# Optimization experiments

Hardware: AMD Instinct MI355X
Metric: run time of the kernel (lower is better)

Reference implementation:

```python
import jax, jax.numpy as jnp
import numpy as np

K = 20          # args.k (minu=True)
EPS = 1e-5      # BatchNorm eps
BNS = float(1.0 / np.sqrt(1.0 + EPS))  # eval-mode BN with running_mean=0, running_var=1


def knn_idx(x, k):
    # x: (B, C, N); returns indices of k nearest neighbors (incl. self): (B, N, k)
    xx = jnp.sum(x * x, axis=1)                       # (B, N)
    inner = jnp.einsum('bcn,bcm->bnm', x, x)          # (B, N, N)
    dist = 2.0 * inner - xx[:, :, None] - xx[:, None, :]  # = -||xi - xj||^2
    return jax.lax.top_k(dist, k)[1]


def graph_feature(x, k):
    # x: (B, C, N) -> edge features (B, 2C, N, k) = cat(neighbor - center, center)
    idx = knn_idx(x, k)                               # (B, N, k)
    xt = jnp.transpose(x, (0, 2, 1))                  # (B, N, C)
    feat = jnp.take_along_axis(xt[:, None, :, :], idx[..., None], axis=2)  # (B, N, k, C)
    center = xt[:, :, None, :]
    out = jnp.concatenate([feat - center, jnp.broadcast_to(center, feat.shape)], axis=-1)
    return jnp.transpose(out, (0, 3, 1, 2))


def edge_block(x, w, g, b, k):
    # EdgeConv: gather -> 1x1 conv -> BN(eval) -> LeakyReLU(0.2) -> max over neighbors
    h = graph_feature(x, k)                           # (B, 2C, N, k)
    y = jnp.einsum('bcnk,oc->bonk', h, w)
    y = g[None, :, None, None] * (y * BNS) + b[None, :, None, None]
    y = jax.nn.leaky_relu(y, 0.2)
    return jnp.max(y, axis=-1)                        # (B, O, N)


def _bn1(v, g, b):
    return g * (v * BNS) + b


def setup_inputs() -> dict:
    key = jax.random.key(0)
    ks = jax.random.split(key, 32)
    B, C, N = 16, 6, 1024

    def w(k_, shape):
        return jax.random.normal(k_, shape, jnp.float32) / np.sqrt(shape[1])

    def gm(k_, n):
        return 1.0 + 0.1 * jax.random.normal(k_, (n,), jnp.float32)

    def bt(k_, n):
        return 0.1 * jax.random.normal(k_, (n,), jnp.float32)

    return {
        'x': jax.random.normal(ks[0], (B, C, N), jnp.float32),
        'disc': jax.random.normal(ks[1], (B, 1), jnp.float32),
        'w1': w(ks[2], (64, 12)),   'g1': gm(ks[3], 64),   'b1': bt(ks[4], 64),
        'w2': w(ks[5], (64, 128)),  'g2': gm(ks[6], 64),   'b2': bt(ks[7], 64),
        'w3': w(ks[8], (128, 128)), 'g3': gm(ks[9], 128),  'b3': bt(ks[10], 128),
        'w4': w(ks[11], (256, 256)),'g4': gm(ks[12], 256), 'b4': bt(ks[13], 256),
        'w5': w(ks[14], (1024, 512)),'g5': gm(ks[15], 1024),'b5': bt(ks[16], 1024),
        'wl1': w(ks[17], (256, 2048)),'g6': gm(ks[18], 256),'b6': bt(ks[19], 256),
        'wl2': w(ks[20], (128, 256)),'g7': gm(ks[21], 128),'b7': bt(ks[22], 128),
        'wl21': w(ks[23], (64, 128)),
        'wl22': w(ks[24], (32, 64)),'g8': gm(ks[25], 32), 'b8': bt(ks[26], 32),
        'wl3': w(ks[27], (90, 32)),
    }


def reference(x, disc, w1, g1, b1, w2, g2, b2, w3, g3, b3, w4, g4, b4,
              w5, g5, b5, wl1, g6, b6, wl2, g7, b7, wl21, wl22, g8, b8, wl3):
    # disc is accepted by the original forward but unused
    x1 = edge_block(x, w1, g1, b1, K)                 # (B, 64, N)
    x2 = edge_block(x1, w2, g2, b2, K)                # (B, 64, N)
    x3 = edge_block(x2, w3, g3, b3, K)                # (B, 128, N)
    x4 = edge_block(x3, w4, g4, b4, K)                # (B, 256, N)
    h = jnp.concatenate([x1, x2, x3, x4], axis=1)     # (B, 512, N)
    y = jnp.einsum('bcn,oc->bon', h, w5)              # conv5 1x1
    y = g5[None, :, None] * (y * BNS) + b5[None, :, None]
    y = jax.nn.leaky_relu(y, 0.2)                     # (B, emb, N)
    p = jnp.concatenate([jnp.max(y, axis=2), jnp.mean(y, axis=2)], axis=1)  # (B, 2*emb)
    z = jax.nn.leaky_relu(_bn1(p @ wl1.T, g6, b6), 0.2)
    z = jax.nn.leaky_relu(_bn1(z @ wl2.T, g7, b7), 0.2)
    z = jax.nn.gelu(_bn1((z @ wl21.T) @ wl22.T, g8, b8), approximate=False)
    return z @ wl3.T                                  # (B, 90)
```

## Files before the change

kernel.cpp:

```cpp
#include <hip/hip_runtime.h>
#include <math.h>
#include <float.h>

#define BNS_C 0.9999950000374996f

typedef __bf16 bf8 __attribute__((ext_vector_type(8)));
typedef float f4 __attribute__((ext_vector_type(4)));
union I4BF8 { int4 i; bf8 b; };

static __device__ __forceinline__ unsigned short f2bf(float f) {
    unsigned u = __float_as_uint(f);
    u += 0x7fff + ((u >> 16) & 1);
    return (unsigned short)(u >> 16);
}

__global__ void k_xin_t(const float* __restrict__ x, float* __restrict__ X0, float* __restrict__ xx) {
    int i = blockIdx.x * 256 + threadIdx.x;
    int b = i >> 10, n = i & 1023;
    const float* xb = x + (((size_t)b * 6) << 10) + n;
    float4* o4 = (float4*)(X0 + ((size_t)i << 3));
    float v0 = xb[0], v1 = xb[1 << 10], v2 = xb[2 << 10];
    float v3 = xb[3 << 10], v4 = xb[4 << 10], v5 = xb[5 << 10];
    o4[0] = make_float4(v0, v1, v2, v3);
    o4[1] = make_float4(v4, v5, 0.f, 0.f);
    xx[i] = v0*v0 + v1*v1 + v2*v2 + v3*v3 + v4*v4 + v5*v5;
}

__global__ __launch_bounds__(256) void k_gram2(const float* __restrict__ X, const float* __restrict__ xx,
                                               float* __restrict__ D, int Cp, int b0) {
    int z = blockIdx.z, b = b0 + z;
    int n0 = blockIdx.y * 64, m0 = blockIdx.x * 64;
    __shared__ float As[32 * 68], Bs[32 * 68];
    int tid = threadIdx.x;
    int ti = tid & 15, tj = tid >> 4;
    float acc[4][4] = {};
    const float* Xb = X + (((size_t)b) << 10) * Cp;
    for (int c0 = 0; c0 < Cp; c0 += 32) {
        for (int e = tid; e < 2048; e += 256) {
            int row = e >> 5, cc = e & 31, c = c0 + cc;
            float a = 0.f, bb = 0.f;
            if (c < Cp) {
                a  = Xb[(size_t)(n0 + row) * Cp + c];
                bb = Xb[(size_t)(m0 + row) * Cp + c];
            }
            As[cc * 68 + row] = a; Bs[cc * 68 + row] = bb;
        }
        __syncthreads();
#pragma unroll 8
        for (int cc = 0; cc < 32; ++cc) {
            const float4 av = *(const float4*)(As + cc * 68 + 4 * tj);
            const float4 bv = *(const float4*)(Bs + cc * 68 + 4 * ti);
            acc[0][0] += av.x * bv.x; acc[0][1] += av.x * bv.y; acc[0][2] += av.x * bv.z; acc[0][3] += av.x * bv.w;
            acc[1][0] += av.y * bv.x; acc[1][1] += av.y * bv.y; acc[1][2] += av.y * bv.z; acc[1][3] += av.y * bv.w;
            acc[2][0] += av.z * bv.x; acc[2][1] += av.z * bv.y; acc[2][2] += av.z * bv.z; acc[2][3] += av.z * bv.w;
            acc[3][0] += av.w * bv.x; acc[3][1] += av.w * bv.y; acc[3][2] += av.w * bv.z; acc[3][3] += av.w * bv.w;
        }
        __syncthreads();
    }
    const float4 xm = *(const float4*)(xx + (b << 10) + m0 + 4 * ti);
#pragma unroll
    for (int a = 0; a < 4; ++a) {
        int n = n0 + 4 * tj + a;
        float xn = xx[(b << 10) + n];
        float4 o;
        o.x = 2.f * acc[a][0] - xn - xm.x;
        o.y = 2.f * acc[a][1] - xn - xm.y;
        o.z = 2.f * acc[a][2] - xn - xm.z;
        o.w = 2.f * acc[a][3] - xn - xm.w;
        *(float4*)(D + ((size_t)((z << 10) + n) << 10) + m0 + 4 * ti) = o;
    }
}

__global__ __launch_bounds__(256) void k_topk(const float* __restrict__ D, int* __restrict__ idxo, int b0) {
    const int K = 20;
    int lane = threadIdx.x & 63;
    int rl = blockIdx.x * 4 + (threadIdx.x >> 6);
    const float* row = D + ((size_t)rl << 10);
    float d[16];
#pragma unroll
    for (int j = 0; j < 16; ++j) d[j] = row[lane + 64 * j];
    int rg = (b0 << 10) + rl;
    for (int it = 0; it < K; ++it) {
        float bv = d[0]; int bj = 0;
#pragma unroll
        for (int j = 1; j < 16; ++j) if (d[j] > bv) { bv = d[j]; bj = j; }
        int bm = lane + (bj << 6);
        for (int off = 32; off > 0; off >>= 1) {
            float ov = __shfl_down(bv, off);
            int   om = __shfl_down(bm, off);
            if (ov > bv || (ov == bv && om < bm)) { bv = ov; bm = om; }
        }
        bm = __shfl(bm, 0);
        if (lane == 0) idxo[rg * K + it] = bm;
        if ((bm & 63) == lane) d[bm >> 6] = -FLT_MAX;
    }
}

__global__ __launch_bounds__(256) void k_uv(const float* __restrict__ X, const float* __restrict__ w,
                                            float* __restrict__ V, float* __restrict__ U,
                                            int Cp, int C, int O) {
    int n0 = blockIdx.x * 64, o0 = blockIdx.y * 64, b = blockIdx.z;
    __shared__ float Xs[32 * 68], Was[32 * 68], Wds[32 * 68];
    int tid = threadIdx.x, ti = tid & 15, tj = tid >> 4;
    float accv[4][4] = {}, accu[4][4] = {};
    const float* Xb = X + (((size_t)b) << 10) * Cp;
    int W2 = 2 * C;
    for (int c0 = 0; c0 < Cp; c0 += 32) {
        for (int e = tid; e < 2048; e += 256) {
            int row = e >> 5, cc = e & 31, c = c0 + cc;
            Xs[cc * 68 + row] = (c < Cp) ? Xb[(size_t)(n0 + row) * Cp + c] : 0.f;
            float wa = 0.f, wd = 0.f;
            if (c < C) {
                float a_ = w[(size_t)(o0 + row) * W2 + c];
                float b_ = w[(size_t)(o0 + row) * W2 + C + c];
                wa = a_; wd = b_ - a_;
            }
            Was[cc * 68 + row] = wa; Wds[cc * 68 + row] = wd;
        }
        __syncthreads();
#pragma unroll 8
        for (int cc = 0; cc < 32; ++cc) {
            const float4 xv = *(const float4*)(Xs  + cc * 68 + 4 * tj);
            const float4 av = *(const float4*)(Was + cc * 68 + 4 * ti);
            const float4 dv = *(const float4*)(Wds + cc * 68 + 4 * ti);
            accv[0][0] += xv.x * av.x; accv[0][1] += xv.x * av.y; accv[0][2] += xv.x * av.z; accv[0][3] += xv.x * av.w;
            accv[1][0] += xv.y * av.x; accv[1][1] += xv.y * av.y; accv[1][2] += xv.y * av.z; accv[1][3] += xv.y * av.w;
            accv[2][0] += xv.z * av.x; accv[2][1] += xv.z * av.y; accv[2][2] += xv.z * av.z; accv[2][3] += xv.z * av.w;
            accv[3][0] += xv.w * av.x; accv[3][1] += xv.w * av.y; accv[3][2] += xv.w * av.z; accv[3][3] += xv.w * av.w;
            accu[0][0] += xv.x * dv.x; accu[0][1] += xv.x * dv.y; accu[0][2] += xv.x * dv.z; accu[0][3] += xv.x * dv.w;
            accu[1][0] += xv.y * dv.x; accu[1][1] += xv.y * dv.y; accu[1][2] += xv.y * dv.z; accu[1][3] += xv.y * dv.w;
            accu[2][0] += xv.z * dv.x; accu[2][1] += xv.z * dv.y; accu[2][2] += xv.z * dv.z; accu[2][3] += xv.z * dv.w;
            accu[3][0] += xv.w * dv.x; accu[3][1] += xv.w * dv.y; accu[3][2] += xv.w * dv.z; accu[3][3] += xv.w * dv.w;
        }
        __syncthreads();
    }
#pragma unroll
    for (int a = 0; a < 4; ++a) {
        int n = n0 + 4 * tj + a;
        size_t base = ((size_t)((b << 10) + n)) * O + o0 + 4 * ti;
        *(float4*)(V + base) = make_float4(accv[a][0], accv[a][1], accv[a][2], accv[a][3]);
        *(float4*)(U + base) = make_float4(accu[a][0], accu[a][1], accu[a][2], accu[a][3]);
    }
}

__global__ __launch_bounds__(256) void k_gmax(const float* __restrict__ V, const float* __restrict__ U,
                                              const int* __restrict__ idx,
                                              const float* __restrict__ gg, const float* __restrict__ bb,
                                              float* __restrict__ Xo, float* __restrict__ xx,
                                              unsigned short* __restrict__ HB, int coff, int O) {
    __shared__ float sxx[4];
    int tid = threadIdx.x;
    int Tn = 256 / O;
    int j = tid / O, o = tid - j * O;
    int pt = blockIdx.x * Tn + j;
    int b = pt >> 10, n = pt & 1023;
    float uv = U[(size_t)pt * O + o];
    float gv = gg[o], bv = bb[o];
    const int* ip = idx + (size_t)pt * 20;
    float mx = -FLT_MAX;
    for (int k = 0; k < 20; ++k) {
        int m = ip[k] & 1023;
        float vv = V[(size_t)((b << 10) + m) * O + o];
        float y = gv * ((vv + uv) * BNS_C) + bv;
        y = y > 0.f ? y : 0.2f * y;
        mx = fmaxf(mx, y);
    }
    Xo[(size_t)pt * O + o] = mx;
    int c = coff + o;
    HB[(((size_t)(b * 16 + (c >> 5)) << 10) + n) * 32 + (c & 31)] = f2bf(mx);
    float s = mx * mx;
#pragma unroll
    for (int off = 32; off; off >>= 1) s += __shfl_down(s, off);
    int wid = tid >> 6, lane = tid & 63;
    if (lane == 0) sxx[wid] = s;
    __syncthreads();
    if (o == 0) {
        int Wpp = O >> 6;
        float t = 0.f;
        for (int w = 0; w < Wpp; ++w) t += sxx[j * Wpp + w];
        xx[pt] = t;
    }
}

__global__ __launch_bounds__(256) void k_final_mfma(const unsigned short* __restrict__ HB,
                                                    const float* __restrict__ w5,
                                                    const float* __restrict__ g5,
                                                    const float* __restrict__ b5,
                                                    float* __restrict__ pp) {
    int b = blockIdx.x;
    int nt = blockIdx.z;
    int wv = threadIdx.x >> 6, lane = threadIdx.x & 63;
    int r = lane & 15, q = lane >> 4;
    int o = blockIdx.y * 64 + wv * 16 + r;
    bf8 Bfr[16];
    const float* wrow = w5 + (size_t)o * 512 + q * 8;
#pragma unroll
    for (int s = 0; s < 16; ++s) {
        float4 f0 = *(const float4*)(wrow + s * 32);
        float4 f1 = *(const float4*)(wrow + s * 32 + 4);
        I4BF8 u_;
        u_.i.x = f2bf(f0.x) | ((unsigned)f2bf(f0.y) << 16);
        u_.i.y = f2bf(f0.z) | ((unsigned)f2bf(f0.w) << 16);
        u_.i.z = f2bf(f1.x) | ((unsigned)f2bf(f1.y) << 16);
        u_.i.w = f2bf(f1.z) | ((unsigned)f2bf(f1.w) << 16);
        Bfr[s] = u_.b;
    }
    float gb = g5[o] * BNS_C, bv = b5[o];
    float mx = -FLT_MAX, sm = 0.f;
    for (int g = 0; g < 4; ++g) {
        int row0 = (nt << 8) + (g << 6);
        f4 C0 = {0.f, 0.f, 0.f, 0.f}, C1 = C0, C2 = C0, C3 = C0;
#pragma unroll
        for (int s = 0; s < 16; ++s) {
            const unsigned short* slab = HB + (((size_t)(b * 16 + s) << 10) + row0) * 32 + q * 8;
            I4BF8 A0, A1, A2, A3;
            A0.i = *(const int4*)(slab + (size_t)( 0 + r) * 32);
            A1.i = *(const int4*)(slab + (size_t)(16 + r) * 32);
            A2.i = *(const int4*)(slab + (size_t)(32 + r) * 32);
            A3.i = *(const int4*)(slab + (size_t)(48 + r) * 32);
            C0 = __builtin_amdgcn_mfma_f32_16x16x32_bf16(A0.b, Bfr[s], C0, 0, 0, 0);
            C1 = __builtin_amdgcn_mfma_f32_16x16x32_bf16(A1.b, Bfr[s], C1, 0, 0, 0);
            C2 = __builtin_amdgcn_mfma_f32_16x16x32_bf16(A2.b, Bfr[s], C2, 0, 0, 0);
            C3 = __builtin_amdgcn_mfma_f32_16x16x32_bf16(A3.b, Bfr[s], C3, 0, 0, 0);
        }
#pragma unroll
        for (int e = 0; e < 4; ++e) {
            float y0 = gb * C0[e] + bv; y0 = y0 > 0.f ? y0 : 0.2f * y0; mx = fmaxf(mx, y0); sm += y0;
            float y1 = gb * C1[e] + bv; y1 = y1 > 0.f ? y1 : 0.2f * y1; mx = fmaxf(mx, y1); sm += y1;
            float y2 = gb * C2[e] + bv; y2 = y2 > 0.f ? y2 : 0.2f * y2; mx = fmaxf(mx, y2); sm += y2;
            float y3 = gb * C3[e] + bv; y3 = y3 > 0.f ? y3 : 0.2f * y3; mx = fmaxf(mx, y3); sm += y3;
        }
    }
    mx = fmaxf(mx, __shfl_down(mx, 32)); sm += __shfl_down(sm, 32);
    mx = fmaxf(mx, __shfl_down(mx, 16)); sm += __shfl_down(sm, 16);
    if (q == 0) {
        float* pb = pp + (size_t)(nt * 16 + b) * 2048;
        pb[o] = mx;
        pb[1024 + o] = sm;
    }
}

__global__ __launch_bounds__(256) void k_fc2p(const float* __restrict__ pp, const float* __restrict__ w,
                                              const float* __restrict__ gg, const float* __restrict__ bb,
                                              float* __restrict__ out, int O) {
    int gw = blockIdx.x * 4 + (threadIdx.x >> 6);
    int lane = threadIdx.x & 63;
    int r = gw / O, o = gw - r * O;
    const float* wr = w + (size_t)o * 2048;
    float s = 0.f;
    for (int c = lane; c < 2048; c += 64) {
        const float* q0 = pp + (size_t)r * 2048 + c;
        float v;
        if (c < 1024) {
            v = fmaxf(fmaxf(q0[0], q0[16 * 2048]), fmaxf(q0[32 * 2048], q0[48 * 2048]));
        } else {
            v = (q0[0] + q0[16 * 2048] + q0[32 * 2048] + q0[48 * 2048]) * (1.f / 1024.f);
        }
        s += v * wr[c];
    }
#pragma unroll
    for (int off = 32; off; off >>= 1) s += __shfl_down(s, off);
    if (lane == 0) {
        float y = gg[o] * (s * BNS_C) + bb[o];
        out[gw] = y > 0.f ? y : 0.2f * y;
    }
}

__global__ __launch_bounds__(256) void k_fc_tail(const float* __restrict__ z1,
                                                 const float* __restrict__ wl2, const float* __restrict__ g7, const float* __restrict__ b7,
                                                 const float* __restrict__ wl21,
                                                 const float* __restrict__ wl22, const float* __restrict__ g8, const float* __restrict__ b8,
                                                 const float* __restrict__ wl3,
                                                 float* __restrict__ out) {
    __shared__ float L1[128], L2[64], L3[32];
    int r = blockIdx.x;
    int tid = threadIdx.x, lane = tid & 63, wv = tid >> 6;
    const float* ir = z1 + r * 256;
    float a0 = ir[lane], a1 = ir[lane + 64], a2 = ir[lane + 128], a3 = ir[lane + 192];
    for (int ob = 0; ob < 32; ob += 2) {
        int o0 = wv * 32 + ob, o1 = o0 + 1;
        const float* w0 = wl2 + (size_t)o0 * 256;
        const float* w1 = wl2 + (size_t)o1 * 256;
        float s0 = a0 * w0[lane] + a1 * w0[lane + 64] + a2 * w0[lane + 128] + a3 * w0[lane + 192];
        float s1 = a0 * w1[lane] + a1 * w1[lane + 64] + a2 * w1[lane + 128] + a3 * w1[lane + 192];
#pragma unroll
        for (int off = 32; off; off >>= 1) { s0 += __shfl_down(s0, off); s1 += __shfl_down(s1, off); }
        if (lane == 0) {
            float y0 = g7[o0] * (s0 * BNS_C) + b7[o0]; L1[o0] = y0 > 0.f ? y0 : 0.2f * y0;
            float y1 = g7[o1] * (s1 * BNS_C) + b7[o1]; L1[o1] = y1 > 0.f ? y1 : 0.2f * y1;
        }
    }
    __syncthreads();
    float b0v = L1[lane], b1v = L1[lane + 64];
    for (int ob = 0; ob < 16; ob += 2) {
        int o0 = wv * 16 + ob, o1 = o0 + 1;
        const float* w0 = wl21 + (size_t)o0 * 128;
        const float* w1 = wl21 + (size_t)o1 * 128;
        float s0 = b0v * w0[lane] + b1v * w0[lane + 64];
        float s1 = b0v * w1[lane] + b1v * w1[lane + 64];
#pragma unroll
        for (int off = 32; off; off >>= 1) { s0 += __shfl_down(s0, off); s1 += __shfl_down(s1, off); }
        if (lane == 0) { L2[o0] = s0; L2[o1] = s1; }
    }
    __syncthreads();
    float c0v = L2[lane];
    for (int ob = 0; ob < 8; ob += 2) {
        int o0 = wv * 8 + ob, o1 = o0 + 1;
        float s0 = c0v * wl22[(size_t)o0 * 64 + lane];
        float s1 = c0v * wl22[(size_t)o1 * 64 + lane];
#pragma unroll
        for (int off = 32; off; off >>= 1) { s0 += __shfl_down(s0, off); s1 += __shfl_down(s1, off); }
        if (lane == 0) {
            float y0 = g8[o0] * (s0 * BNS_C) + b8[o0];
            L3[o0] = 0.5f * y0 * (1.f + erff(y0 * 0.70710678118654752f));
            float y1 = g8[o1] * (s1 * BNS_C) + b8[o1];
            L3[o1] = 0.5f * y1 * (1.f + erff(y1 * 0.70710678118654752f));
        }
    }
    __syncthreads();
    float d0v = (lane < 32) ? L3[lane] : 0.f;
    for (int o = wv; o < 90; o += 4) {
        float s = (lane < 32) ? d0v * wl3[(size_t)o * 32 + lane] : 0.f;
#pragma unroll
        for (int off = 32; off; off >>= 1) s += __shfl_down(s, off);
        if (lane == 0) out[r * 90 + o] = s;
    }
}

extern "C" void kernel_launch(void* const* d_in, const int* in_sizes, int n_in,
                              void* d_out, int out_size, void* d_ws, size_t ws_size,
                              hipStream_t stream) {
    typedef const float* fp;
    fp x  = (fp)d_in[0];
    fp w1 = (fp)d_in[2],  g1 = (fp)d_in[3],  b1 = (fp)d_in[4];
    fp w2 = (fp)d_in[5],  g2 = (fp)d_in[6],  b2 = (fp)d_in[7];
    fp w3 = (fp)d_in[8],  g3 = (fp)d_in[9],  b3 = (fp)d_in[10];
    fp w4 = (fp)d_in[11], g4 = (fp)d_in[12], b4 = (fp)d_in[13];
    fp w5 = (fp)d_in[14], g5 = (fp)d_in[15], b5 = (fp)d_in[16];
    fp wl1 = (fp)d_in[17], g6 = (fp)d_in[18], b6 = (fp)d_in[19];
    fp wl2 = (fp)d_in[20], g7 = (fp)d_in[21], b7 = (fp)d_in[22];
    fp wl21 = (fp)d_in[23], wl22 = (fp)d_in[24];
    fp g8 = (fp)d_in[25], b8 = (fp)d_in[26], wl3 = (fp)d_in[27];

    char* ws = (char*)d_ws;
    size_t off = 0;
    auto alloc = [&](size_t floats) { float* p_ = (float*)(ws + off); off += floats * 4; off = (off + 255) & ~(size_t)255; return p_; };
    float* X0  = alloc(131072);
    float* X1  = alloc(1048576);
    float* X2  = alloc(1048576);
    float* X3  = alloc(2097152);
    float* X4  = alloc(4194304);
    float* xx  = alloc(16384);
    int*   nbr = (int*)alloc(327680);
    unsigned short* HB = (unsigned short*)alloc(4194304);
    float* pp  = alloc(131072);
    float* z1  = alloc(4096);
    size_t poolAvail = (ws_size > off) ? (ws_size - off) / 4 : 0;
    int fullD = poolAvail >= 16777216;
    float* pool = alloc(fullD ? 16777216 : 8388608);

    float* D = pool;
    float* V = pool;
    float* U = pool + 4194304;

    k_xin_t<<<64, 256, 0, stream>>>(x, X0, xx);

    struct Blk { const float* Xin; int Cp, C, O, coff; const float *w, *g, *b; float* Xout; };
    Blk blks[4] = {
        {X0, 8,   6,   64,  0,   w1, g1, b1, X1},
        {X1, 64,  64,  64,  64,  w2, g2, b2, X2},
        {X2, 64,  64,  128, 128, w3, g3, b3, X3},
        {X3, 128, 128, 256, 256, w4, g4, b4, X4},
    };
    for (int i = 0; i < 4; ++i) {
        const Blk& B_ = blks[i];
        if (fullD) {
            k_gram2<<<dim3(16, 16, 16), 256, 0, stream>>>(B_.Xin, xx, D, B_.Cp, 0);
            k_topk<<<4096, 256, 0, stream>>>(D, nbr, 0);
        } else {
            for (int b0 = 0; b0 < 16; b0 += 8) {
                k_gram2<<<dim3(16, 16, 8), 256, 0, stream>>>(B_.Xin, xx, D, B_.Cp, b0);
                k_topk<<<2048, 256, 0, stream>>>(D, nbr, b0);
            }
        }
        k_uv<<<dim3(16, B_.O / 64, 16), 256, 0, stream>>>(B_.Xin, B_.w, V, U, B_.Cp, B_.C, B_.O);
        int Tn = 256 / B_.O;
        k_gmax<<<16384 / Tn, 256, 0, stream>>>(V, U, nbr, B_.g, B_.b, B_.Xout, xx, HB, B_.coff, B_.O);
    }

    k_final_mfma<<<dim3(16, 16, 4), 256, 0, stream>>>(HB, w5, g5, b5, pp);

    k_fc2p<<<(16 * 256) / 4, 256, 0, stream>>>(pp, wl1, g6, b6, z1, 256);
    k_fc_tail<<<16, 256, 0, stream>>>(z1, wl2, g7, b7, wl21, wl22, g8, b8, wl3, (float*)d_out);
}
```

Baseline: 939.0 us.

## Replace iterative argmax top-k with per-lane sorted lists and packed-key merge

The top-k kernel now packs each distance and its inverted index into one sortable 64-bit key. Each lane sorts its 16 keys with a sorting network and stores the sorted column in shared memory, so each of the 20 selection rounds needs only a wave max-reduction over the lanes' current heads. This drops the 16-element scan per round and the separate tie-break compare on the index. In exchange it adds a one-time sort, 32 KB of shared memory per block, and 64-bit shuffles, which could lower occupancy.

```diff
diff --git a/kernel.cpp b/kernel.cpp
--- a/kernel.cpp
+++ b/kernel.cpp
@@ -71,30 +71,54 @@
     }
 }
 
+#define CE(I,J) { if (kk[I] < kk[J]) { unsigned long long t_ = kk[I]; kk[I] = kk[J]; kk[J] = t_; } }
 __global__ __launch_bounds__(256) void k_topk(const float* __restrict__ D, int* __restrict__ idxo, int b0) {
-    const int K = 20;
-    int lane = threadIdx.x & 63;
-    int rl = blockIdx.x * 4 + (threadIdx.x >> 6);
+    __shared__ unsigned long long H[4096];
+    int lane = threadIdx.x & 63, wv = threadIdx.x >> 6;
+    int rl = blockIdx.x * 4 + wv;
     const float* row = D + ((size_t)rl << 10);
-    float d[16];
-#pragma unroll
-    for (int j = 0; j < 16; ++j) d[j] = row[lane + 64 * j];
-    int rg = (b0 << 10) + rl;
-    for (int it = 0; it < K; ++it) {
-        float bv = d[0]; int bj = 0;
-#pragma unroll
-        for (int j = 1; j < 16; ++j) if (d[j] > bv) { bv = d[j]; bj = j; }
-        int bm = lane + (bj << 6);
-        for (int off = 32; off > 0; off >>= 1) {
-            float ov = __shfl_down(bv, off);
-            int   om = __shfl_down(bm, off);
-            if (ov > bv || (ov == bv && om < bm)) { bv = ov; bm = om; }
-        }
-        bm = __shfl(bm, 0);
-        if (lane == 0) idxo[rg * K + it] = bm;
-        if ((bm & 63) == lane) d[bm >> 6] = -FLT_MAX;
-    }
-}
+    unsigned long long kk[16];
+#pragma unroll
+    for (int j = 0; j < 16; ++j) {
+        float v = row[lane + 64 * j];
+        unsigned u = __float_as_uint(v);
+        unsigned s = u ^ ((unsigned)(((int)u) >> 31) | 0x80000000u);
+        int m = lane + (j << 6);
+        kk[j] = ((unsigned long long)s << 32) | (unsigned)(1023 - m);
+    }
+    CE(0,1) CE(2,3) CE(0,2) CE(1,3) CE(1,2)
+    CE(4,5) CE(6,7) CE(4,6) CE(5,7) CE(5,6)
+    CE(0,4) CE(2,6) CE(2,4) CE(1,5) CE(3,7) CE(3,5) CE(1,2) CE(3,4) CE(5,6)
+    CE(8,9) CE(10,11) CE(8,10) CE(9,11) CE(9,10)
+    CE(12,13) CE(14,15) CE(12,14) CE(13,15) CE(13,14)
+    CE(8,12) CE(10,14) CE(10,12) CE(9,13) CE(11,15) CE(11,13) CE(9,10) CE(11,12) CE(13,14)
+    CE(0,8) CE(4,12) CE(4,8) CE(2,10) CE(6,14) CE(6,10) CE(2,4) CE(6,8) CE(10,12)
+    CE(1,9) CE(5,13) CE(5,9) CE(3,11) CE(7,15) CE(7,11) CE(3,5) CE(7,9) CE(11,13)
+    CE(1,2) CE(3,4) CE(5,6) CE(7,8) CE(9,10) CE(11,12) CE(13,14)
+    unsigned long long* Hw = H + (wv << 10);
+#pragma unroll
+    for (int j = 0; j < 16; ++j) Hw[(j << 6) + lane] = kk[j];
+    int ptr = 0;
+    unsigned long long h = kk[0];
+    int* outp = idxo + (size_t)((b0 << 10) + rl) * 20;
+    for (int it = 0; it < 20; ++it) {
+        unsigned long long bk = h;
+#pragma unroll
+        for (int off = 32; off; off >>= 1) {
+            unsigned long long ok = __shfl_down(bk, off);
+            if (ok > bk) bk = ok;
+        }
+        unsigned wlo = __builtin_amdgcn_readfirstlane((unsigned)bk);
+        unsigned whi = __builtin_amdgcn_readfirstlane((unsigned)(bk >> 32));
+        unsigned long long win = ((unsigned long long)whi << 32) | wlo;
+        if (lane == 0) outp[it] = 1023 - (int)(wlo & 1023);
+        if (h == win) {
+            ++ptr;
+            h = (ptr < 16) ? Hw[(ptr << 6) + lane] : 0ULL;
+        }
+    }
+}
+#undef CE
 
 __global__ __launch_bounds__(256) void k_uv(const float* __restrict__ X, const float* __restrict__ w,
                                             float* __restrict__ V, float* __restrict__ U,
```

Result: faster. 837.4 us, median of 2 (-10.8%).
